# Performance work log

Hardware: AMD Instinct MI355X
Metric: run time of the kernel (lower is better)

The kernel has to match this reference:

```python
import jax, jax.numpy as jnp
import numpy as np

BETA = 0.25  # commitment cost (init kwarg)


def setup_inputs() -> dict:
    key = jax.random.key(0)
    k1, k2 = jax.random.split(key)
    B, C, H, W = 8, 256, 64, 64
    K = 8192  # codebook_size
    z = jax.random.normal(k1, (B, C, H, W), dtype=jnp.float32)
    # torch init is uniform(-1/K, 1/K); use same scale
    codebook = jax.random.uniform(k2, (K, C), dtype=jnp.float32,
                                  minval=-1.0 / K, maxval=1.0 / K)
    return {"z": z, "codebook": codebook}


def reference(z, codebook):
    # z: [B, C, H, W] -> [B, H, W, C]
    z_bhwc = jnp.transpose(z, (0, 2, 3, 1))
    D = codebook.shape[1]
    zf = z_bhwc.reshape(-1, D)  # [N, D]
    # squared euclidean distances: ||z||^2 + ||e||^2 - 2 z.e  -> [N, K]
    d = (jnp.sum(zf * zf, axis=1, keepdims=True)
         + jnp.sum(codebook * codebook, axis=1)
         - 2.0 * jnp.einsum('nd,kd->nk', zf, codebook))
    min_encoding_indices = jnp.argmin(d, axis=1)  # [N]
    z_q = codebook[min_encoding_indices].reshape(z_bhwc.shape)  # [B,H,W,C]
    sg = jax.lax.stop_gradient
    # legacy=False branch
    loss = (BETA * jnp.mean((sg(z_q) - z_bhwc) ** 2)
            + jnp.mean((z_q - sg(z_bhwc)) ** 2))
    # straight-through estimator
    z_q = z_bhwc + sg(z_q - z_bhwc)
    z_q = jnp.transpose(z_q, (0, 3, 1, 2))  # back to [B, C, H, W]
    return z_q, loss, min_encoding_indices
```

## Files before the change

### kernel.cpp

```cpp
#include <hip/hip_runtime.h>
#include <hip/hip_bf16.h>
#include <math.h>

typedef unsigned short u16;
typedef unsigned int u32;
typedef unsigned long long u64;
typedef __attribute__((ext_vector_type(8))) _Float16 f16x8;
typedef __attribute__((ext_vector_type(4))) float f32x4;

#define B_   8
#define C_   256
#define HW_  4096
#define N_   32768
#define K_   8192

#define O_LOSSP 0ULL
#define O_E2    16384ULL
#define O_ZN2   49152ULL
#define O_IDX   180224ULL
#define O_ZT    311296ULL
#define O_AP    33865728ULL
#define O_BP    50642944ULL
#define O_CAND  54837248ULL
#define WS_NEED 88391680ULL

#define THRESH_T 9e-5f

#define GSWZ(r) (((r) >> 1) & 3)

__device__ __forceinline__ u16 f2h(float f) {
    _Float16 h = (_Float16)f;
    return __builtin_bit_cast(u16, h);
}

__device__ __forceinline__ void gload16(const void* g, void* l) {
    __builtin_amdgcn_global_load_lds((const __attribute__((address_space(1))) void*)g,
                                     (__attribute__((address_space(3))) void*)l, 16, 0, 0);
}


__global__ __launch_bounds__(256) void vq_prep_z(const float* __restrict__ z,
                                                 float* __restrict__ zT,
                                                 u16* __restrict__ Ap,
                                                 float* __restrict__ zn2g) {
    __shared__ float zl[128][65];
    const int tid = threadIdx.x;
    const int bb = blockIdx.x >> 6;
    const int hwc = blockIdx.x & 63;
    const int hw0 = hwc * 64;
    const int n0 = bb * HW_ + hw0;
    const int lane = tid & 63, wid = tid >> 6;
    const int r = tid >> 2;
    const int u4 = tid & 3;
    const int n = n0 + r;
    const int r7 = n & 127;
    double zacc = 0.0;

    for (int h = 0; h < 2; ++h) {
        __syncthreads();
        for (int c0 = 0; c0 < 128; c0 += 4) {
            int c = c0 + (tid >> 6);
            zl[c][tid & 63] = z[((size_t)(bb * C_ + h * 128 + c)) * HW_ + hw0 + (tid & 63)];
        }
        __syncthreads();
        for (int it = 0; it < 8; ++it) {
            int rp = it * 8 + wid * 2 + (lane >> 5);
            int c4 = (lane & 31) * 4;
            float4 v = { zl[c4][rp], zl[c4 + 1][rp], zl[c4 + 2][rp], zl[c4 + 3][rp] };
            *(float4*)(zT + (size_t)(n0 + rp) * C_ + h * 128 + c4) = v;
        }
        #pragma unroll
        for (int q = 0; q < 4; ++q) {
            u16 tmp[8];
            #pragma unroll
            for (int j = 0; j < 8; ++j) {
                float f = zl[q * 32 + u4 * 8 + j][r];
                zacc += (double)f * (double)f;
                tmp[j] = f2h(f);
            }
            char* dst = (char*)Ap + ((size_t)((n >> 7) * 8 + h * 4 + q)) * 8192
                      + r7 * 64 + ((u4 * 16) ^ (GSWZ(r7) << 4));
            *(uint4*)dst = *(uint4*)tmp;
        }
    }
    zacc += __shfl_xor(zacc, 1);
    zacc += __shfl_xor(zacc, 2);
    if (u4 == 0) zn2g[n] = (float)zacc;
}

__global__ __launch_bounds__(256) void vq_prep_cb(const float* __restrict__ cb,
                                                  u16* __restrict__ Bp,
                                                  float* __restrict__ e2g) {
    const int tid = threadIdx.x;
    const int k0 = blockIdx.x * 64;
    const int r = tid >> 2;
    const int u4 = tid & 3;
    const int k = k0 + r;
    const int r7 = k & 127;
    double eacc = 0.0;
    #pragma unroll
    for (int kc8 = 0; kc8 < 8; ++kc8) {
        const float* src = cb + (size_t)k * C_ + kc8 * 32 + u4 * 8;
        float4 v0 = *(const float4*)(src);
        float4 v1 = *(const float4*)(src + 4);
        float vals[8] = { v0.x, v0.y, v0.z, v0.w, v1.x, v1.y, v1.z, v1.w };
        u16 tmp[8];
        #pragma unroll
        for (int j = 0; j < 8; ++j) {
            eacc += (double)vals[j] * (double)vals[j];
            tmp[j] = f2h(vals[j] * 8192.0f);
        }
        char* dst = (char*)Bp + ((size_t)((k >> 7) * 8 + kc8)) * 8192
                  + r7 * 64 + ((u4 * 16) ^ (GSWZ(r7) << 4));
        *(uint4*)dst = *(uint4*)tmp;
    }
    eacc += __shfl_xor(eacc, 1);
    eacc += __shfl_xor(eacc, 2);
    if (u4 == 0) e2g[k] = (float)eacc;
}

__global__ __launch_bounds__(256) void vq_gemm_top2(const u16* __restrict__ Ap,
                                                    const u16* __restrict__ Bp,
                                                    u32* __restrict__ cand) {
    __shared__ char lds[32768];
    const int tid = threadIdx.x;
    const int lane = tid & 63, wid = tid >> 6;
    const int wm = wid >> 1, wn = wid & 1;
    const int l15 = lane & 15, l4 = lane >> 4;

    const int raw = blockIdx.x;
    const int m_tile = raw >> 6;
    const int n_tile = (raw & 7) * 8 + ((raw >> 3) & 7);

    f32x4 acc[4][4];
    #pragma unroll
    for (int i = 0; i < 4; ++i)
        #pragma unroll
        for (int j = 0; j < 4; ++j) acc[i][j] = (f32x4){0.f, 0.f, 0.f, 0.f};

    int rc[4], rz[4], xc[4], xz[4];
    #pragma unroll
    for (int f = 0; f < 4; ++f) {
        rc[f] = wm * 64 + f * 16 + l15;
        rz[f] = wn * 64 + f * 16 + l15;
        xc[f] = GSWZ(rc[f]) << 4;
        xz[f] = GSWZ(rz[f]) << 4;
    }
    const int ob = l4 * 16;

    const char* codes_src = (const char*)Bp + (size_t)n_tile * 65536;
    const char* z_src     = (const char*)Ap + (size_t)m_tile * 65536;

    #define STAGE(buf, kc)                                                        \
        do {                                                                      \
            const char* cs_ = codes_src + (size_t)(kc) * 8192;                    \
            const char* zs_ = z_src + (size_t)(kc) * 8192;                        \
            char* lb_ = lds + (buf) * 16384;                                      \
            gload16(cs_ + tid * 16, lb_ + tid * 16);                              \
            gload16(cs_ + 4096 + tid * 16, lb_ + 4096 + tid * 16);                \
            gload16(zs_ + tid * 16, lb_ + 8192 + tid * 16);                       \
            gload16(zs_ + 4096 + tid * 16, lb_ + 12288 + tid * 16);               \
        } while (0)

    #define COMPUTE(buf)                                                          \
        do {                                                                      \
            const char* base_ = lds + (buf) * 16384;                              \
            f16x8 la[4], lb[4];                                                   \
            _Pragma("unroll")                                                     \
            for (int f = 0; f < 4; ++f) {                                         \
                la[f] = *(const f16x8*)(base_ + rc[f] * 64 + (ob ^ xc[f]));       \
                lb[f] = *(const f16x8*)(base_ + 8192 + rz[f] * 64 + (ob ^ xz[f]));\
            }                                                                     \
            _Pragma("unroll")                                                     \
            for (int fm = 0; fm < 4; ++fm)                                        \
                _Pragma("unroll")                                                 \
                for (int fn = 0; fn < 4; ++fn)                                    \
                    acc[fm][fn] = __builtin_amdgcn_mfma_f32_16x16x32_f16(         \
                        la[fm], lb[fn], acc[fm][fn], 0, 0, 0);                    \
        } while (0)

    STAGE(0, 0);
    #pragma unroll
    for (int kc = 0; kc < 8; ++kc) {
        __syncthreads();
        if (kc < 7) STAGE((kc + 1) & 1, kc + 1);
        COMPUTE(kc & 1);
    }

    #undef STAGE
    #undef COMPUTE

    const int ktile = n_tile * 2 + wm;
    #pragma unroll
    for (int fn = 0; fn < 4; ++fn) {
        u32 m1 = 0xFFFFFFFFu, m2 = 0xFFFFFFFFu;
        #pragma unroll
        for (int fm = 0; fm < 4; ++fm) {
            #pragma unroll
            for (int rv = 0; rv < 4; ++rv) {
                float w = fmaf(acc[fm][fn][rv], -0x1p-12f, 0.5f);
                u32 p = (__float_as_uint(w) & ~63u) | (u32)(fm * 16 + l4 * 4 + rv);
                u32 t = m1 > p ? m1 : p;
                m1 = m1 < p ? m1 : p;
                m2 = m2 < t ? m2 : t;
            }
        }
        #pragma unroll
        for (int off = 16; off <= 32; off <<= 1) {
            u32 b1 = __shfl_xor(m1, off);
            u32 b2 = __shfl_xor(m2, off);
            u32 t = m1 > b1 ? m1 : b1;
            m1 = m1 < b1 ? m1 : b1;
            u32 s2 = m2 < b2 ? m2 : b2;
            m2 = s2 < t ? s2 : t;
        }
        if (l4 == 0) {
            int rowg = m_tile * 128 + wn * 64 + fn * 16 + l15;
            *(uint2*)(cand + (size_t)rowg * 256 + ktile * 2) = make_uint2(m1, m2);
        }
    }
}

__global__ __launch_bounds__(256) void vq_pick(const u32* __restrict__ cand,
                                               const float* __restrict__ zT,
                                               const float* __restrict__ cb,
                                               const float* __restrict__ e2g,
                                               const float* __restrict__ zn2g,
                                               int* __restrict__ idxg,
                                               float* __restrict__ out) {
    const int lane = threadIdx.x & 63, wid = threadIdx.x >> 6;
    const int row = blockIdx.x * 4 + wid;
    const uint4 e = ((const uint4*)(cand + (size_t)row * 256))[lane];
    u32 m = e.x < e.y ? e.x : e.y;
    u32 mzw = e.z < e.w ? e.z : e.w;
    m = m < mzw ? m : mzw;
    #pragma unroll
    for (int off = 32; off >= 1; off >>= 1) {
        u32 o = __shfl_xor(m, off);
        m = o < m ? o : m;
    }
    const float thr = __uint_as_float(m & ~63u) + THRESH_T;
    const u32 ev[4] = { e.x, e.y, e.z, e.w };
    u64 msk[4];
    int tot = 0;
    #pragma unroll
    for (int j = 0; j < 4; ++j) {
        msk[j] = __ballot(__uint_as_float(ev[j] & ~63u) <= thr);
        tot += __popcll((unsigned long long)msk[j]);
    }
    int bk;
    if (tot == 1) {
        const int j = msk[0] ? 0 : (msk[1] ? 1 : (msk[2] ? 2 : 3));
        const int l = __ffsll((unsigned long long)msk[j]) - 1;
        const u32 val = __shfl(ev[j], l);
        bk = ((l * 4 + j) >> 1) * 64 + (int)(val & 63u);
    } else {
        const float4 zv = *(const float4*)(zT + (size_t)row * C_ + lane * 4);
        const float zn2a = zn2g[row];
        float bd = INFINITY;
        bk = 0x7fffffff;
        #pragma unroll
        for (int j = 0; j < 4; ++j) {
            u64 mj = msk[j];
            while (mj) {
                const int l = __ffsll((unsigned long long)mj) - 1;
                mj &= mj - 1;
                const u32 val = __shfl(ev[j], l);
                const int k = ((l * 4 + j) >> 1) * 64 + (int)(val & 63u);
                const float4 cv = *(const float4*)(cb + (size_t)k * C_ + lane * 4);
                double s = (double)zv.x * cv.x + (double)zv.y * cv.y
                         + (double)zv.z * cv.z + (double)zv.w * cv.w;
                #pragma unroll
                for (int off = 32; off >= 1; off >>= 1) s += __shfl_xor(s, off);
                const float sf = (float)s;
                const float d = (zn2a + e2g[k]) - 2.0f * sf;
                if (d < bd || (d == bd && k < bk)) { bd = d; bk = k; }
            }
        }
    }
    if (lane == 0) {
        idxg[row] = bk;
        out[8388609 + row] = (float)bk;
    }
}

__global__ __launch_bounds__(256) void vq_zq_loss_kernel(const float* __restrict__ z,
                                                         const float* __restrict__ cb,
                                                         const int* __restrict__ idxg,
                                                         float* __restrict__ out,
                                                         double* __restrict__ partial) {
    double acc = 0.0;
    for (size_t i4 = (size_t)blockIdx.x * 256 + threadIdx.x; i4 < 2097152ULL;
         i4 += 2048ULL * 256ULL) {
        const size_t i = i4 * 4;
        const int hw = (int)(i & 4095);
        const int bc = (int)(i >> 12);
        const int c = bc & 255;
        const int b = bc >> 8;
        const int n = (b << 12) + hw;
        const float4 zv = *(const float4*)(z + i);
        const int k0 = idxg[n], k1 = idxg[n + 1], k2 = idxg[n + 2], k3 = idxg[n + 3];
        const float t0 = cb[(size_t)k0 * C_ + c] - zv.x;
        const float t1 = cb[(size_t)k1 * C_ + c] - zv.y;
        const float t2 = cb[(size_t)k2 * C_ + c] - zv.z;
        const float t3 = cb[(size_t)k3 * C_ + c] - zv.w;
        float4 o = { zv.x + t0, zv.y + t1, zv.z + t2, zv.w + t3 };
        *(float4*)(out + i) = o;
        acc += (double)t0 * t0 + (double)t1 * t1 + (double)t2 * t2 + (double)t3 * t3;
    }
    #pragma unroll
    for (int off = 32; off >= 1; off >>= 1) acc += __shfl_xor(acc, off);
    __shared__ double ls[4];
    const int lane = threadIdx.x & 63, wid = threadIdx.x >> 6;
    if (lane == 0) ls[wid] = acc;
    __syncthreads();
    if (threadIdx.x == 0) partial[blockIdx.x] = ls[0] + ls[1] + ls[2] + ls[3];
}

__global__ __launch_bounds__(256) void vq_loss_final(const double* __restrict__ partial,
                                                     float* __restrict__ out) {
    double acc = 0.0;
    for (int j = threadIdx.x; j < 2048; j += 256) acc += partial[j];
    #pragma unroll
    for (int off = 32; off >= 1; off >>= 1) acc += __shfl_xor(acc, off);
    __shared__ double ls[4];
    const int lane = threadIdx.x & 63, wid = threadIdx.x >> 6;
    if (lane == 0) ls[wid] = acc;
    __syncthreads();
    if (threadIdx.x == 0)
        out[8388608] = (float)(1.25 * (ls[0] + ls[1] + ls[2] + ls[3]) / 8388608.0);
}

__global__ __launch_bounds__(256) void vq_e2_old(const float* __restrict__ cb,
                                                 float* __restrict__ e2g) {
    int lane = threadIdx.x & 63;
    int w = threadIdx.x >> 6;
    int k = blockIdx.x * 4 + w;
    const float4 v = *reinterpret_cast<const float4*>(cb + (size_t)k * C_ + lane * 4);
    double acc = (double)v.x * v.x + (double)v.y * v.y
               + (double)v.z * v.z + (double)v.w * v.w;
    #pragma unroll
    for (int off = 32; off >= 1; off >>= 1) acc += __shfl_xor(acc, off);
    if (lane == 0) e2g[k] = (float)acc;
}

__global__ __launch_bounds__(256) void vq_zn2_old(const float* __restrict__ z,
                                                  float* __restrict__ zn2g) {
    int n = blockIdx.x * 256 + threadIdx.x;
    int b = n >> 12;
    int hw = n & 4095;
    const float* p = z + (size_t)b * C_ * HW_ + hw;
    double acc = 0.0;
    #pragma unroll 8
    for (int c = 0; c < C_; ++c) {
        float v = p[(size_t)c * HW_];
        acc += (double)v * (double)v;
    }
    zn2g[n] = (float)acc;
}

__global__ __launch_bounds__(256) void vq_argmin_old(const float* __restrict__ z,
                                                     const float* __restrict__ cb,
                                                     const float* __restrict__ e2g,
                                                     const float* __restrict__ zn2g,
                                                     int* __restrict__ idxg) {
    __shared__ float zt[C_][32];
    __shared__ float et[64][64];
    const int tid = threadIdx.x;
    const int n0 = blockIdx.x * 32;
    const int b = n0 >> 12;
    const int hw0 = n0 & 4095;
    {
        const int nn = tid & 31;
        const int c8 = tid >> 5;
        #pragma unroll
        for (int j = 0; j < 32; ++j) {
            const int c = j * 8 + c8;
            zt[c][nn] = z[(size_t)(b * C_ + c) * HW_ + hw0 + nn];
        }
    }
    const int cg = tid & 15;
    const int rg = tid >> 4;
    const int r0 = rg * 2;
    __syncthreads();
    const float zn2a = zn2g[n0 + r0];
    const float zn2b = zn2g[n0 + r0 + 1];
    float dmin0 = INFINITY, dmin1 = INFINITY;
    int imin0 = 0, imin1 = 0;
    const int kk = tid >> 2;
    const int c4 = (tid & 3) * 16;
    for (int kt = 0; kt < K_; kt += 64) {
        double s00 = 0, s01 = 0, s02 = 0, s03 = 0;
        double s10 = 0, s11 = 0, s12 = 0, s13 = 0;
        for (int cc = 0; cc < C_; cc += 64) {
            __syncthreads();
            {
                const float* src = cb + (size_t)(kt + kk) * C_ + cc + c4;
                #pragma unroll
                for (int j = 0; j < 16; j += 4) {
                    const float4 v = *reinterpret_cast<const float4*>(src + j);
                    et[c4 + j + 0][kk] = v.x;
                    et[c4 + j + 1][kk] = v.y;
                    et[c4 + j + 2][kk] = v.z;
                    et[c4 + j + 3][kk] = v.w;
                }
            }
            __syncthreads();
            #pragma unroll 4
            for (int c2 = 0; c2 < 64; ++c2) {
                const float2 zv = *reinterpret_cast<const float2*>(&zt[cc + c2][r0]);
                const float4 ev = *reinterpret_cast<const float4*>(&et[c2][cg * 4]);
                const double z0 = (double)zv.x, z1 = (double)zv.y;
                s00 += z0 * ev.x; s01 += z0 * ev.y; s02 += z0 * ev.z; s03 += z0 * ev.w;
                s10 += z1 * ev.x; s11 += z1 * ev.y; s12 += z1 * ev.z; s13 += z1 * ev.w;
            }
        }
        const int kbase = kt + cg * 4;
        const float sf0[4] = {(float)s00, (float)s01, (float)s02, (float)s03};
        const float sf1[4] = {(float)s10, (float)s11, (float)s12, (float)s13};
        #pragma unroll
        for (int j = 0; j < 4; ++j) {
            const int k = kbase + j;
            const float e2k = e2g[k];
            const float d0 = (zn2a + e2k) - 2.0f * sf0[j];
            const float d1 = (zn2b + e2k) - 2.0f * sf1[j];
            if (d0 < dmin0) { dmin0 = d0; imin0 = k; }
            if (d1 < dmin1) { dmin1 = d1; imin1 = k; }
        }
    }
    #pragma unroll
    for (int off = 8; off >= 1; off >>= 1) {
        const float od0 = __shfl_xor(dmin0, off);
        const int   oi0 = __shfl_xor(imin0, off);
        const float od1 = __shfl_xor(dmin1, off);
        const int   oi1 = __shfl_xor(imin1, off);
        if (od0 < dmin0 || (od0 == dmin0 && oi0 < imin0)) { dmin0 = od0; imin0 = oi0; }
        if (od1 < dmin1 || (od1 == dmin1 && oi1 < imin1)) { dmin1 = od1; imin1 = oi1; }
    }
    if (cg == 0) {
        idxg[n0 + r0]     = imin0;
        idxg[n0 + r0 + 1] = imin1;
    }
}

__global__ __launch_bounds__(256) void vq_final_old(const int* __restrict__ idxg,
                                                    float* __restrict__ out) {
    const int i = blockIdx.x * 256 + threadIdx.x;
    out[8388609 + i] = (float)idxg[i];
}

extern "C" void kernel_launch(void* const* d_in, const int* in_sizes, int n_in,
                              void* d_out, int out_size, void* d_ws, size_t ws_size,
                              hipStream_t stream) {
    const float* z  = (const float*)d_in[0];
    const float* cb = (const float*)d_in[1];
    float* out = (float*)d_out;
    char* ws = (char*)d_ws;

    double* lossp = (double*)(ws + O_LOSSP);
    float*  e2g  = (float*)(ws + O_E2);
    float*  zn2g = (float*)(ws + O_ZN2);
    int*    idxg = (int*)(ws + O_IDX);

    if (ws_size >= WS_NEED) {
        float* zT   = (float*)(ws + O_ZT);
        u16*   Ap   = (u16*)(ws + O_AP);
        u16*   Bp   = (u16*)(ws + O_BP);
        u32*   cand = (u32*)(ws + O_CAND);

        hipLaunchKernelGGL(vq_prep_cb, dim3(128), dim3(256), 0, stream, cb, Bp, e2g);
        hipLaunchKernelGGL(vq_prep_z, dim3(512), dim3(256), 0, stream, z, zT, Ap, zn2g);
        hipLaunchKernelGGL(vq_gemm_top2, dim3(16384), dim3(256), 0, stream, Ap, Bp, cand);
        hipLaunchKernelGGL(vq_pick, dim3(N_ / 4), dim3(256), 0, stream,
                           cand, zT, cb, e2g, zn2g, idxg, out);
    } else {
        hipLaunchKernelGGL(vq_e2_old, dim3(K_ / 4), dim3(256), 0, stream, cb, e2g);
        hipLaunchKernelGGL(vq_zn2_old, dim3(N_ / 256), dim3(256), 0, stream, z, zn2g);
        hipLaunchKernelGGL(vq_argmin_old, dim3(N_ / 32), dim3(256), 0, stream,
                           z, cb, e2g, zn2g, idxg);
        hipLaunchKernelGGL(vq_final_old, dim3(N_ / 256), dim3(256), 0, stream, idxg, out);
    }

    hipLaunchKernelGGL(vq_zq_loss_kernel, dim3(2048), dim3(256), 0, stream,
                       z, cb, idxg, out, lossp);
    hipLaunchKernelGGL(vq_loss_final, dim3(1), dim3(256), 0, stream, lossp, out);
}
```

Baseline: 223.6 us.

## Merge prep kernels and deepen GEMM load pipeline with explicit waitcnt barriers

Combines the codebook and z preparation kernels into one launch of 640 blocks, with the first 128 blocks handling the codebook, which saves one kernel launch and lets both run concurrently. In the GEMM kernel, the first two K-stages are now prefetched up front, and the single __syncthreads is replaced by explicit s_waitcnt vmcnt/lgkmcnt plus s_barrier with sched_barrier fences. This keeps one async global->LDS load in flight while computing the other buffer. The hand-tuned vmcnt counts depend on how many loads STAGE issues, and a wrong count would be a correctness risk.

```diff
diff --git a/kernel.cpp b/kernel.cpp
--- a/kernel.cpp
+++ b/kernel.cpp
@@ -39,14 +39,48 @@
 }
 
 
-__global__ __launch_bounds__(256) void vq_prep_z(const float* __restrict__ z,
-                                                 float* __restrict__ zT,
-                                                 u16* __restrict__ Ap,
-                                                 float* __restrict__ zn2g) {
+__global__ __launch_bounds__(256) void vq_prep(const float* __restrict__ z,
+                                               const float* __restrict__ cb,
+                                               float* __restrict__ zT,
+                                               u16* __restrict__ Ap,
+                                               u16* __restrict__ Bp,
+                                               float* __restrict__ zn2g,
+                                               float* __restrict__ e2g) {
     __shared__ float zl[128][65];
     const int tid = threadIdx.x;
-    const int bb = blockIdx.x >> 6;
-    const int hwc = blockIdx.x & 63;
+
+    if (blockIdx.x < 128) {
+        const int k0 = blockIdx.x * 64;
+        const int r = tid >> 2;
+        const int u4 = tid & 3;
+        const int k = k0 + r;
+        const int r7 = k & 127;
+        double eacc = 0.0;
+        #pragma unroll
+        for (int kc8 = 0; kc8 < 8; ++kc8) {
+            const float* src = cb + (size_t)k * C_ + kc8 * 32 + u4 * 8;
+            float4 v0 = *(const float4*)(src);
+            float4 v1 = *(const float4*)(src + 4);
+            float vals[8] = { v0.x, v0.y, v0.z, v0.w, v1.x, v1.y, v1.z, v1.w };
+            u16 tmp[8];
+            #pragma unroll
+            for (int j = 0; j < 8; ++j) {
+                eacc += (double)vals[j] * (double)vals[j];
+                tmp[j] = f2h(vals[j] * 8192.0f);
+            }
+            char* dst = (char*)Bp + ((size_t)((k >> 7) * 8 + kc8)) * 8192
+                      + r7 * 64 + ((u4 * 16) ^ (GSWZ(r7) << 4));
+            *(uint4*)dst = *(uint4*)tmp;
+        }
+        eacc += __shfl_xor(eacc, 1);
+        eacc += __shfl_xor(eacc, 2);
+        if (u4 == 0) e2g[k] = (float)eacc;
+        return;
+    }
+
+    const int bidz = blockIdx.x - 128;
+    const int bb = bidz >> 6;
+    const int hwc = bidz & 63;
     const int hw0 = hwc * 64;
     const int n0 = bb * HW_ + hw0;
     const int lane = tid & 63, wid = tid >> 6;
@@ -86,37 +120,6 @@
     zacc += __shfl_xor(zacc, 1);
     zacc += __shfl_xor(zacc, 2);
     if (u4 == 0) zn2g[n] = (float)zacc;
-}
-
-__global__ __launch_bounds__(256) void vq_prep_cb(const float* __restrict__ cb,
-                                                  u16* __restrict__ Bp,
-                                                  float* __restrict__ e2g) {
-    const int tid = threadIdx.x;
-    const int k0 = blockIdx.x * 64;
-    const int r = tid >> 2;
-    const int u4 = tid & 3;
-    const int k = k0 + r;
-    const int r7 = k & 127;
-    double eacc = 0.0;
-    #pragma unroll
-    for (int kc8 = 0; kc8 < 8; ++kc8) {
-        const float* src = cb + (size_t)k * C_ + kc8 * 32 + u4 * 8;
-        float4 v0 = *(const float4*)(src);
-        float4 v1 = *(const float4*)(src + 4);
-        float vals[8] = { v0.x, v0.y, v0.z, v0.w, v1.x, v1.y, v1.z, v1.w };
-        u16 tmp[8];
-        #pragma unroll
-        for (int j = 0; j < 8; ++j) {
-            eacc += (double)vals[j] * (double)vals[j];
-            tmp[j] = f2h(vals[j] * 8192.0f);
-        }
-        char* dst = (char*)Bp + ((size_t)((k >> 7) * 8 + kc8)) * 8192
-                  + r7 * 64 + ((u4 * 16) ^ (GSWZ(r7) << 4));
-        *(uint4*)dst = *(uint4*)tmp;
-    }
-    eacc += __shfl_xor(eacc, 1);
-    eacc += __shfl_xor(eacc, 2);
-    if (u4 == 0) e2g[k] = (float)eacc;
 }
 
 __global__ __launch_bounds__(256) void vq_gemm_top2(const u16* __restrict__ Ap,
@@ -179,16 +182,30 @@
                         la[fm], lb[fn], acc[fm][fn], 0, 0, 0);                    \
         } while (0)
 
+    #define FENCE() __builtin_amdgcn_sched_barrier(0)
+
     STAGE(0, 0);
+    STAGE(1, 1);
     #pragma unroll
     for (int kc = 0; kc < 8; ++kc) {
-        __syncthreads();
-        if (kc < 7) STAGE((kc + 1) & 1, kc + 1);
+        if (kc < 7) { asm volatile("s_waitcnt vmcnt(4)" ::: "memory"); }
+        else        { asm volatile("s_waitcnt vmcnt(0)" ::: "memory"); }
+        FENCE();
+        __builtin_amdgcn_s_barrier();
+        FENCE();
         COMPUTE(kc & 1);
+        if (kc < 6) {
+            asm volatile("s_waitcnt lgkmcnt(0)" ::: "memory");
+            FENCE();
+            __builtin_amdgcn_s_barrier();
+            FENCE();
+            STAGE(kc & 1, kc + 2);
+        }
     }
 
     #undef STAGE
     #undef COMPUTE
+    #undef FENCE
 
     const int ktile = n_tile * 2 + wm;
     #pragma unroll
@@ -468,8 +485,8 @@
         u16*   Bp   = (u16*)(ws + O_BP);
         u32*   cand = (u32*)(ws + O_CAND);
 
-        hipLaunchKernelGGL(vq_prep_cb, dim3(128), dim3(256), 0, stream, cb, Bp, e2g);
-        hipLaunchKernelGGL(vq_prep_z, dim3(512), dim3(256), 0, stream, z, zT, Ap, zn2g);
+        hipLaunchKernelGGL(vq_prep, dim3(640), dim3(256), 0, stream,
+                           z, cb, zT, Ap, Bp, zn2g, e2g);
         hipLaunchKernelGGL(vq_gemm_top2, dim3(16384), dim3(256), 0, stream, Ap, Bp, cand);
         hipLaunchKernelGGL(vq_pick, dim3(N_ / 4), dim3(256), 0, stream,
                            cand, zT, cb, e2g, zn2g, idxg, out);
```

Result: no change. 223.8 us (+0.1%).
